# Performance work log

Measured on AMD Instinct MI355X. Metric: run time of the kernel, lower is better.

The kernel has to match this reference:

```python
import jax, jax.numpy as jnp
import numpy as np

LATENT_DIM = 32
INPUT_DIM = 16
N_UNITS = 20
N_TRAJ = 4096
T = 512


def setup_inputs() -> dict:
    key = jax.random.key(0)
    ks = jax.random.split(key, 8)
    cat_dim = LATENT_DIM + INPUT_DIM
    s1 = 1.0 / np.sqrt(cat_dim)
    s2 = 1.0 / np.sqrt(N_UNITS)
    return {
        "data": jax.random.normal(ks[0], (N_TRAJ, T, INPUT_DIM), dtype=jnp.float32),
        "time_steps": jnp.arange(T, dtype=jnp.float32),
        "Wu1": jax.random.normal(ks[1], (cat_dim, N_UNITS), dtype=jnp.float32) * s1,
        "bu1": jnp.zeros((N_UNITS,), dtype=jnp.float32),
        "Wu2": jax.random.normal(ks[2], (N_UNITS, LATENT_DIM), dtype=jnp.float32) * s2,
        "bu2": jnp.zeros((LATENT_DIM,), dtype=jnp.float32),
        "Wr1": jax.random.normal(ks[3], (cat_dim, N_UNITS), dtype=jnp.float32) * s1,
        "br1": jnp.zeros((N_UNITS,), dtype=jnp.float32),
        "Wr2": jax.random.normal(ks[4], (N_UNITS, LATENT_DIM), dtype=jnp.float32) * s2,
        "br2": jnp.zeros((LATENT_DIM,), dtype=jnp.float32),
        "Wn1": jax.random.normal(ks[5], (cat_dim, N_UNITS), dtype=jnp.float32) * s1,
        "bn1": jnp.zeros((N_UNITS,), dtype=jnp.float32),
        "Wn2": jax.random.normal(ks[6], (N_UNITS, LATENT_DIM), dtype=jnp.float32) * s2,
        "bn2": jnp.zeros((LATENT_DIM,), dtype=jnp.float32),
    }


def _mlp(h, W1, b1, W2, b2):
    # 2-layer MLP with tanh hidden, linear out
    return jnp.tanh(h @ W1 + b1) @ W2 + b2


def reference(data, time_steps, Wu1, bu1, Wu2, bu2, Wr1, br1, Wr2, br2, Wn1, bn1, Wn2, bn2):
    n_traj = data.shape[0]
    latent_dim = Wu2.shape[1]

    def step(prev_y, xi):
        yc = jnp.concatenate([prev_y, xi], axis=-1)            # [B, L+D]
        u = jax.nn.sigmoid(_mlp(yc, Wu1, bu1, Wu2, bu2))       # update gate
        r = jax.nn.sigmoid(_mlp(yc, Wr1, br1, Wr2, br2))       # reset gate
        cc = jnp.concatenate([prev_y * r, xi], axis=-1)
        n = jnp.tanh(_mlp(cc, Wn1, bn1, Wn2, bn2))             # candidate state
        new_y = (1.0 - u) * n + u * prev_y
        return new_y, new_y

    prev_y = jnp.zeros((n_traj, latent_dim), dtype=data.dtype)
    xs = jnp.swapaxes(data, 0, 1)                              # [T, B, D]
    yi, ys = jax.lax.scan(step, prev_y, xs)
    latent_ys = jnp.swapaxes(ys, 0, 1)                         # [B, T, L]
    return yi, latent_ys
```

## Files before the change

kernel.cpp:

```cpp
#include <hip/hip_runtime.h>

#define T_STEPS 512
#define NTRAJ   4096
#define LAT     32
#define INPD    16
#define HID     20
#define CAT     48

__device__ __forceinline__ float fast_tanh(float x) {
    float e = __expf(2.0f * x);
    float r = __builtin_amdgcn_rcpf(e + 1.0f);
    return fmaf(-2.0f, r, 1.0f);
}
__device__ __forceinline__ float fast_sigmoid(float x) {
    float e = __expf(-x);
    return __builtin_amdgcn_rcpf(e + 1.0f);
}

#define FMAC_DPP(acc, ring, w, I) \
    asm("v_fmac_f32_dpp %0, %1, %2 row_ror:" #I " row_mask:0xf bank_mask:0xf" \
        : "+v"(acc) : "v"(ring), "v"(w))

#define REP15(M) M(1) M(2) M(3) M(4) M(5) M(6) M(7) M(8) \
                 M(9) M(10) M(11) M(12) M(13) M(14) M(15)

__global__ __launch_bounds__(256, 2) void rnn_fused(
    const float* __restrict__ data,
    const float* __restrict__ Wu1, const float* __restrict__ bu1,
    const float* __restrict__ Wu2, const float* __restrict__ bu2,
    const float* __restrict__ Wr1, const float* __restrict__ br1,
    const float* __restrict__ Wr2, const float* __restrict__ br2,
    const float* __restrict__ Wn1, const float* __restrict__ bn1,
    const float* __restrict__ Wn2, const float* __restrict__ bn2,
    float* __restrict__ out_yi, float* __restrict__ out_lat)
{
    const int tid  = threadIdx.x;
    const int w    = tid >> 6;
    const int lane = tid & 63;
    const int c    = lane & 31;
    const int g    = lane >> 5;
    const int p    = (lane >> 4) & 1;
    const int b    = (blockIdx.x << 2) + w;

    const float* W1 = g ? Wr1 : Wu1;
    const float* B1 = g ? br1 : bu1;
    const float* W2 = g ? Wr2 : Wu2;
    const float* B2 = g ? br2 : bu2;
    const bool realc = (c < HID);

    float wa_a[16], wa_b[16], wa_x[16], wb_a[16], wb_b[16];
    float wc_a[16], wc_b[16], wc_x[16], wd_a[16], wd_b[16];
    #pragma unroll
    for (int i = 0; i < 16; ++i) {
        int s  = (c - i) & 15;
        int sa = 16 * p + s;
        int sb = 16 * (1 - p) + s;
        int sx = 32 + s;
        wa_a[i] = realc ? W1[sa * HID + c] : 0.0f;
        wa_b[i] = realc ? W1[sb * HID + c] : 0.0f;
        wa_x[i] = realc ? W1[sx * HID + c] : 0.0f;
        wb_a[i] = (sa < HID) ? W2[sa * LAT + c] : 0.0f;
        wb_b[i] = (sb < HID) ? W2[sb * LAT + c] : 0.0f;
        wc_a[i] = realc ? Wn1[sa * HID + c] : 0.0f;
        wc_b[i] = realc ? Wn1[sb * HID + c] : 0.0f;
        wc_x[i] = realc ? Wn1[sx * HID + c] : 0.0f;
        wd_a[i] = (sa < HID) ? Wn2[sa * LAT + c] : 0.0f;
        wd_b[i] = (sb < HID) ? Wn2[sb * LAT + c] : 0.0f;
    }
    const float ba = realc ? B1[c] : 0.0f;
    const float bb = B2[c];
    const float bc = realc ? bn1[c] : 0.0f;
    const float bd = bn2[c];

    const float* xptr = data + (size_t)b * T_STEPS * INPD + (lane & 15);
    float x0 = xptr[0];
    float x1 = xptr[INPD];

    float y  = 0.0f;
    float y2 = 0.0f;
    float* olat = out_lat + (size_t)b * T_STEPS * LAT + c;

    for (int t = 0; t < T_STEPS; ++t) {
        int tf = t + 2; tf = (tf < T_STEPS) ? tf : (T_STEPS - 1);
        float xn = xptr[(size_t)tf * INPD];

        float acc[4] = {ba, 0.f, 0.f, 0.f};
        acc[0] = fmaf(y,  wa_a[0], acc[0]);
        acc[1] = fmaf(y2, wa_b[0], acc[1]);
        acc[2] = fmaf(x0, wa_x[0], acc[2]);
        #define PA(i) \
            FMAC_DPP(acc[(i)&3],     y,  wa_a[(i)], i); \
            FMAC_DPP(acc[((i)+1)&3], y2, wa_b[(i)], i); \
            FMAC_DPP(acc[((i)+2)&3], x0, wa_x[(i)], i);
        REP15(PA)
        #undef PA
        float h1 = fast_tanh((acc[0] + acc[1]) + (acc[2] + acc[3]));
        float h2 = __shfl_xor(h1, 16);

        float bcc[4] = {bb, 0.f, 0.f, 0.f};
        bcc[0] = fmaf(h1, wb_a[0], bcc[0]);
        bcc[1] = fmaf(h2, wb_b[0], bcc[1]);
        #define PB(i) \
            FMAC_DPP(bcc[(i)&3],     h1, wb_a[(i)], i); \
            FMAC_DPP(bcc[((i)+1)&3], h2, wb_b[(i)], i);
        REP15(PB)
        #undef PB
        float gate = fast_sigmoid((bcc[0] + bcc[1]) + (bcc[2] + bcc[3]));

        float exch  = __shfl_xor(gate, 32);
        float u_all = g ? exch : gate;
        float r_all = g ? gate : exch;
        float ry    = r_all * y;
        float ry2   = __shfl_xor(ry, 16);

        float ccc[4] = {bc, 0.f, 0.f, 0.f};
        ccc[0] = fmaf(ry,  wc_a[0], ccc[0]);
        ccc[1] = fmaf(ry2, wc_b[0], ccc[1]);
        ccc[2] = fmaf(x0,  wc_x[0], ccc[2]);
        #define PC(i) \
            FMAC_DPP(ccc[(i)&3],     ry,  wc_a[(i)], i); \
            FMAC_DPP(ccc[((i)+1)&3], ry2, wc_b[(i)], i); \
            FMAC_DPP(ccc[((i)+2)&3], x0,  wc_x[(i)], i);
        REP15(PC)
        #undef PC
        float hn  = fast_tanh((ccc[0] + ccc[1]) + (ccc[2] + ccc[3]));
        float hn2 = __shfl_xor(hn, 16);

        float dcc[4] = {bd, 0.f, 0.f, 0.f};
        dcc[0] = fmaf(hn,  wd_a[0], dcc[0]);
        dcc[1] = fmaf(hn2, wd_b[0], dcc[1]);
        #define PD(i) \
            FMAC_DPP(dcc[(i)&3],     hn,  wd_a[(i)], i); \
            FMAC_DPP(dcc[((i)+1)&3], hn2, wd_b[(i)], i);
        REP15(PD)
        #undef PD
        float n = fast_tanh((dcc[0] + dcc[1]) + (dcc[2] + dcc[3]));

        float ny = fmaf(u_all, y - n, n);
        y  = ny;
        y2 = __shfl_xor(ny, 16);
        if (lane < 32) olat[(size_t)t * LAT] = ny;

        x0 = x1; x1 = xn;
    }

    if (lane < 32) out_yi[(size_t)b * LAT + c] = y;
}

extern "C" void kernel_launch(void* const* d_in, const int* in_sizes, int n_in,
                              void* d_out, int out_size, void* d_ws, size_t ws_size,
                              hipStream_t stream) {
    const float* data = (const float*)d_in[0];
    const float* Wu1 = (const float*)d_in[2];
    const float* bu1 = (const float*)d_in[3];
    const float* Wu2 = (const float*)d_in[4];
    const float* bu2 = (const float*)d_in[5];
    const float* Wr1 = (const float*)d_in[6];
    const float* br1 = (const float*)d_in[7];
    const float* Wr2 = (const float*)d_in[8];
    const float* br2 = (const float*)d_in[9];
    const float* Wn1 = (const float*)d_in[10];
    const float* bn1 = (const float*)d_in[11];
    const float* Wn2 = (const float*)d_in[12];
    const float* bn2 = (const float*)d_in[13];

    float* out_yi  = (float*)d_out;
    float* out_lat = out_yi + (size_t)NTRAJ * LAT;

    rnn_fused<<<NTRAJ / 4, 256, 0, stream>>>(
        data, Wu1, bu1, Wu2, bu2, Wr1, br1, Wr2, br2, Wn1, bn1, Wn2, bn2,
        out_yi, out_lat);
}
```

Baseline: 1.153 ms.

## Use permlane swap instructions for cross-lane exchange and launch one wave per block

Replaces the __shfl_xor calls (which go through ds_bpermute in LDS) with v_permlane16_swap and v_permlane32_swap register-level exchanges, selecting the swapped half per lane. It also changes the launch to one 64-thread block per trajectory with launch bounds (64,1) instead of 4 waves per block. The goal is to cut the latency of the serial per-step shuffles on the recurrent critical path. The launch-bounds change may alter register allocation and occupancy, and the s_nop hazard padding adds a little overhead.

After: 1.173 ms. Within noise of the previous version (+1.7%).

```diff
diff --git a/kernel.cpp b/kernel.cpp
--- a/kernel.cpp
+++ b/kernel.cpp
@@ -21,10 +21,21 @@
     asm("v_fmac_f32_dpp %0, %1, %2 row_ror:" #I " row_mask:0xf bank_mask:0xf" \
         : "+v"(acc) : "v"(ring), "v"(w))
 
+__device__ __forceinline__ float swap16(float v, bool podd) {
+    float a = v, b = v;
+    asm("s_nop 1\n\tv_permlane16_swap_b32 %0, %1" : "+v"(a), "+v"(b));
+    return podd ? a : b;
+}
+__device__ __forceinline__ float swap32(float v, bool ghi) {
+    float a = v, b = v;
+    asm("s_nop 1\n\tv_permlane32_swap_b32 %0, %1" : "+v"(a), "+v"(b));
+    return ghi ? a : b;
+}
+
 #define REP15(M) M(1) M(2) M(3) M(4) M(5) M(6) M(7) M(8) \
                  M(9) M(10) M(11) M(12) M(13) M(14) M(15)
 
-__global__ __launch_bounds__(256, 2) void rnn_fused(
+__global__ __launch_bounds__(64, 1) void rnn_fused(
     const float* __restrict__ data,
     const float* __restrict__ Wu1, const float* __restrict__ bu1,
     const float* __restrict__ Wu2, const float* __restrict__ bu2,
@@ -34,13 +45,13 @@
     const float* __restrict__ Wn2, const float* __restrict__ bn2,
     float* __restrict__ out_yi, float* __restrict__ out_lat)
 {
-    const int tid  = threadIdx.x;
-    const int w    = tid >> 6;
-    const int lane = tid & 63;
+    const int lane = threadIdx.x & 63;
     const int c    = lane & 31;
     const int g    = lane >> 5;
     const int p    = (lane >> 4) & 1;
-    const int b    = (blockIdx.x << 2) + w;
+    const int b    = blockIdx.x;
+    const bool podd = (p != 0);
+    const bool ghi  = (g != 0);
 
     const float* W1 = g ? Wr1 : Wu1;
     const float* B1 = g ? br1 : bu1;
@@ -95,7 +106,7 @@
         REP15(PA)
         #undef PA
         float h1 = fast_tanh((acc[0] + acc[1]) + (acc[2] + acc[3]));
-        float h2 = __shfl_xor(h1, 16);
+        float h2 = swap16(h1, podd);
 
         float bcc[4] = {bb, 0.f, 0.f, 0.f};
         bcc[0] = fmaf(h1, wb_a[0], bcc[0]);
@@ -107,11 +118,11 @@
         #undef PB
         float gate = fast_sigmoid((bcc[0] + bcc[1]) + (bcc[2] + bcc[3]));
 
-        float exch  = __shfl_xor(gate, 32);
+        float exch  = swap32(gate, ghi);
         float u_all = g ? exch : gate;
         float r_all = g ? gate : exch;
         float ry    = r_all * y;
-        float ry2   = __shfl_xor(ry, 16);
+        float ry2   = swap16(ry, podd);
 
         float ccc[4] = {bc, 0.f, 0.f, 0.f};
         ccc[0] = fmaf(ry,  wc_a[0], ccc[0]);
@@ -124,7 +135,7 @@
         REP15(PC)
         #undef PC
         float hn  = fast_tanh((ccc[0] + ccc[1]) + (ccc[2] + ccc[3]));
-        float hn2 = __shfl_xor(hn, 16);
+        float hn2 = swap16(hn, podd);
 
         float dcc[4] = {bd, 0.f, 0.f, 0.f};
         dcc[0] = fmaf(hn,  wd_a[0], dcc[0]);
@@ -138,7 +149,7 @@
 
         float ny = fmaf(u_all, y - n, n);
         y  = ny;
-        y2 = __shfl_xor(ny, 16);
+        y2 = swap16(ny, podd);
         if (lane < 32) olat[(size_t)t * LAT] = ny;
 
         x0 = x1; x1 = xn;
@@ -167,7 +178,7 @@
     float* out_yi  = (float*)d_out;
     float* out_lat = out_yi + (size_t)NTRAJ * LAT;
 
-    rnn_fused<<<NTRAJ / 4, 256, 0, stream>>>(
+    rnn_fused<<<NTRAJ, 64, 0, stream>>>(
         data, Wu1, bu1, Wu2, bu2, Wr1, br1, Wr2, br2, Wn1, bn1, Wn2, bn2,
         out_yi, out_lat);
 }
```
